# Kernel tuning notes

Hardware: AMD Instinct MI355X
Metric: run time of the kernel (lower is better)

Reference implementation:

```python
import jax, jax.numpy as jnp
import numpy as np
from jax import lax

KERNEL = 5  # cv2 np.ones((5,5)) structuring element
EDGE_WEIGHT = 0.1


def _edge_weights(target):
    # target: [B,1,H,W] float. Binary mask -> morphological gradient via
    # max-pool (dilate) and min-pool (erode) with 5x5 window, SAME padding.
    # cv2 pads dilate with -inf and erode with +inf, so padding never
    # creates or removes foreground; reduce_window init values match that.
    b = (target > 0.5).astype(target.dtype)
    win = (1, 1, KERNEL, KERNEL)
    ones = (1, 1, 1, 1)
    dilated = lax.reduce_window(b, jnp.float32(-jnp.inf), lax.max, win, ones, 'SAME')
    eroded = lax.reduce_window(b, jnp.float32(jnp.inf), lax.min, win, ones, 'SAME')
    edge = dilated - eroded
    # Samples with empty masks get edge==0 everywhere, so the per-sample
    # binary_mask.sum()>0 guard in the original is a no-op here.
    return jnp.where(edge > 0, jnp.float32(EDGE_WEIGHT), jnp.float32(1.0))


def setup_inputs() -> dict:
    key = jax.random.key(0)
    k1, k2 = jax.random.split(key)
    shape = (32, 1, 1024, 1024)
    pred = jax.random.normal(k1, shape, dtype=jnp.float32)
    target = jax.random.randint(k2, shape, 0, 2).astype(jnp.float32)
    return {"pred": pred, "target": target}


def reference(pred, target):
    # BCEWithLogitsLoss(reduction='none'): softplus(x) - x*t (stable form)
    loss = jax.nn.softplus(pred) - pred * target
    # Weighting branch only taken when target.max()==1 and target.min()==0
    cond = jnp.logical_and(target.max() == 1.0, target.min() == 0.0)
    weights = _edge_weights(target)
    weights = jnp.where(cond, weights, jnp.float32(1.0))
    return (loss * weights).mean()
```

## Files before the change

kernel.cpp:

```cpp
#include <hip/hip_runtime.h>


#define IMG  1024
#define RPW  8
#define NTOT 33554432.0

typedef unsigned long long u64;

__device__ __forceinline__ u64 shfl64(u64 v, int src) {
    unsigned lo = (unsigned)__shfl((int)(unsigned)(v & 0xffffffffULL), src, 64);
    unsigned hi = (unsigned)__shfl((int)(unsigned)(v >> 32), src, 64);
    return ((u64)hi << 32) | lo;
}
__device__ __forceinline__ u64 bcast64(u64 v, int srcImm) {
    unsigned lo = (unsigned)__builtin_amdgcn_readlane((int)(unsigned)(v & 0xffffffffULL), srcImm);
    unsigned hi = (unsigned)__builtin_amdgcn_readlane((int)(unsigned)(v >> 32), srcImm);
    return ((u64)hi << 32) | lo;
}

__device__ __forceinline__ unsigned encf(float f) {
    unsigned u = __float_as_uint(f);
    return (u & 0x80000000u) ? ~u : (u | 0x80000000u);
}
__device__ __forceinline__ float decf(unsigned e) {
    unsigned u = (e & 0x80000000u) ? (e & 0x7fffffffu) : ~e;
    return __uint_as_float(u);
}

__global__ void bbl_init(double* dws, unsigned* uws) {
    if (threadIdx.x == 0) {
        dws[0] = 0.0; dws[1] = 0.0;
        uws[0] = 0xFFFFFFFFu;
        uws[1] = 0u;
    }
}

__global__ __launch_bounds__(256) void bbl_main(
        const float* __restrict__ pred,
        const float* __restrict__ target,
        double* __restrict__ dws, unsigned* __restrict__ uws) {
    __shared__ float    redS1[4], redSe[4];
    __shared__ unsigned redMn[4], redMx[4];

    const int tid  = threadIdx.x;
    const int lane = tid & 63;
    const int wid  = tid >> 6;
    const int gw   = blockIdx.x * 4 + wid;
    const int img  = gw >> 7;
    const int r0   = (gw & 127) * RPW;
    const size_t base = (size_t)img * IMG * IMG;
    const float* tbase = target + base;
    const float* pbase = pred + base;

    const int w = lane & 15;
    const int k = w & 3;

    float vmin = 3.4e38f, vmax = -3.4e38f;
    float s1 = 0.f, se = 0.f;

    auto loadrow = [&](int gr, bool mm) -> u64 {
        const float4* rp = (const float4*)(tbase + (size_t)gr * IMG);
        u64 myw = 0ULL;
        #pragma unroll
        for (int it = 0; it < 4; ++it) {
            float4 v = rp[it * 64 + lane];
            if (mm) {
                vmin = fminf(vmin, fminf(fminf(v.x, v.y), fminf(v.z, v.w)));
                vmax = fmaxf(vmax, fmaxf(fmaxf(v.x, v.y), fmaxf(v.z, v.w)));
            }
            u64 b0 = __ballot(v.x > 0.5f);
            u64 b1 = __ballot(v.y > 0.5f);
            u64 b2 = __ballot(v.z > 0.5f);
            u64 b3 = __ballot(v.w > 0.5f);
            u64 bw = (k == 0) ? b0 : (k == 1) ? b1 : (k == 2) ? b2 : b3;
            if ((w >> 2) == it) myw = bw;
        }
        return myw;
    };

    u64 q0 = loadrow(max(r0 - 2, 0), false);
    u64 q1 = loadrow(max(r0 - 1, 0), false);
    u64 q2 = loadrow(r0, true);
    u64 q3 = loadrow(r0 + 1, true);

    for (int r = r0; r < r0 + RPW; ++r) {
        const int nr = min(r + 2, IMG - 1);
        u64 q4 = loadrow(nr, r + 2 <= r0 + RPW - 1);

        const float4* pp = (const float4*)(pbase + (size_t)r * IMG);
        float4 p0 = pp[0 * 64 + lane];
        float4 p1 = pp[1 * 64 + lane];
        float4 p2 = pp[2 * 64 + lane];
        float4 p3 = pp[3 * 64 + lane];

        u64 vd = q0 | q1 | q2 | q3 | q4;
        u64 ve = q0 & q1 & q2 & q3 & q4;
        u64 ct = q2;

        u64 hd = vd, he = ve;
        #pragma unroll
        for (int di = 0; di < 4; ++di) {
            const int d = (di < 2) ? di - 2 : di - 1;
            int wp = w + d;
            bool inp = (wp >= 0) && (wp < 16);
            u64 ad = shfl64(vd, wp & 15);
            u64 ae = shfl64(ve, wp & 15);
            ad = inp ? ad : 0ULL;
            ae = inp ? ae : ~0ULL;
            int ws2 = wp + ((d > 0) ? -4 : 4);
            u64 bd = shfl64(vd, ws2 & 15);
            u64 be = shfl64(ve, ws2 & 15);
            int kp = k + d;
            u64 rd, re;
            if (d > 0) {
                u64 wd = (bd >> 1) | (ad << 63);
                u64 we = (be >> 1) | (ae << 63);
                rd = (kp <= 3) ? ad : wd;
                re = (kp <= 3) ? ae : we;
            } else {
                u64 wd = (bd << 1) | (ad >> 63);
                u64 we = (be << 1) | (ae >> 63);
                rd = (kp >= 0) ? ad : wd;
                re = (kp >= 0) ? ae : we;
            }
            hd |= rd; he &= re;
        }
        u64 em = hd & ~he;

        #pragma unroll
        for (int it = 0; it < 4; ++it) {
            float4 p = (it == 0) ? p0 : (it == 1) ? p1 : (it == 2) ? p2 : p3;
            #pragma unroll
            for (int m = 0; m < 4; ++m) {
                u64 ew = bcast64(em, it * 4 + m);
                u64 tw = bcast64(ct, it * 4 + m);
                float x = (m == 0) ? p.x : (m == 1) ? p.y : (m == 2) ? p.z : p.w;
                unsigned tb = (unsigned)(tw >> lane) & 1u;
                unsigned eb = (unsigned)(ew >> lane) & 1u;
                float xt = tb ? x : 0.f;
                float sp = fmaxf(x, 0.f) + __logf(1.f + __expf(-fabsf(x)));
                float loss = sp - xt;
                s1 += loss;
                se += eb ? loss : 0.f;
            }
        }

        q0 = q1; q1 = q2; q2 = q3; q3 = q4;
    }

    for (int off = 32; off > 0; off >>= 1) {
        s1   += __shfl_down(s1, off);
        se   += __shfl_down(se, off);
        vmin  = fminf(vmin, __shfl_down(vmin, off));
        vmax  = fmaxf(vmax, __shfl_down(vmax, off));
    }
    if (lane == 0) {
        redS1[wid] = s1; redSe[wid] = se;
        redMn[wid] = encf(vmin); redMx[wid] = encf(vmax);
    }
    __syncthreads();
    if (tid == 0) {
        float S1 = 0.f, Se = 0.f; unsigned mn = 0xFFFFFFFFu, mx = 0u;
        #pragma unroll
        for (int i = 0; i < 4; ++i) {
            S1 += redS1[i]; Se += redSe[i];
            mn = min(mn, redMn[i]); mx = max(mx, redMx[i]);
        }
        atomicAdd(&dws[0], (double)S1);
        atomicAdd(&dws[1], (double)Se);
        atomicMin(&uws[0], mn);
        atomicMax(&uws[1], mx);
    }
}

__global__ void bbl_fin(const double* __restrict__ dws,
                        const unsigned* __restrict__ uws,
                        float* __restrict__ out) {
    if (threadIdx.x == 0) {
        float fmin = decf(uws[0]);
        float fmax = decf(uws[1]);
        bool cond = (fmax == 1.0f) && (fmin == 0.0f);
        double s = cond ? (dws[0] - 0.9 * dws[1]) : dws[0];
        out[0] = (float)(s / NTOT);
    }
}

extern "C" void kernel_launch(void* const* d_in, const int* in_sizes, int n_in,
                              void* d_out, int out_size, void* d_ws, size_t ws_size,
                              hipStream_t stream) {
    const float* pred   = (const float*)d_in[0];
    const float* target = (const float*)d_in[1];
    double*   dws = (double*)d_ws;
    unsigned* uws = (unsigned*)(dws + 2);
    float*    out = (float*)d_out;

    hipLaunchKernelGGL(bbl_init, dim3(1), dim3(64), 0, stream, dws, uws);
    hipLaunchKernelGGL(bbl_main, dim3(1024), dim3(256), 0, stream,
                       pred, target, dws, uws);
    hipLaunchKernelGGL(bbl_fin, dim3(1), dim3(64), 0, stream, dws, uws, out);
}
```

Before: 313.0 us.

## Split fused loss kernel into mask-pack, edge, and loss passes via workspace

Replaces the single fused kernel, which recomputed five rows of target ballots per output row, with three kernels. The first packs the target into a bitmask in workspace and reduces min/max. The second computes the 5x5 edge bitmask from the packed rows. The third streams pred together with both bitmasks to accumulate the loss. This removes the repeated halo reads of target and the cross-lane shuffles, at the cost of extra kernel launches and small workspace round trips, and keeps the original kernel as a fallback when the workspace is too small.

```diff
diff --git a/kernel.cpp b/kernel.cpp
--- a/kernel.cpp
+++ b/kernel.cpp
@@ -1,22 +1,12 @@
 #include <hip/hip_runtime.h>
 
 
-#define IMG  1024
-#define RPW  8
-#define NTOT 33554432.0
+#define IMG   1024
+#define NTOT  33554432.0
+#define NF4   8388608LL
+#define GRID  2048
 
 typedef unsigned long long u64;
-
-__device__ __forceinline__ u64 shfl64(u64 v, int src) {
-    unsigned lo = (unsigned)__shfl((int)(unsigned)(v & 0xffffffffULL), src, 64);
-    unsigned hi = (unsigned)__shfl((int)(unsigned)(v >> 32), src, 64);
-    return ((u64)hi << 32) | lo;
-}
-__device__ __forceinline__ u64 bcast64(u64 v, int srcImm) {
-    unsigned lo = (unsigned)__builtin_amdgcn_readlane((int)(unsigned)(v & 0xffffffffULL), srcImm);
-    unsigned hi = (unsigned)__builtin_amdgcn_readlane((int)(unsigned)(v >> 32), srcImm);
-    return ((u64)hi << 32) | lo;
-}
 
 __device__ __forceinline__ unsigned encf(float f) {
     unsigned u = __float_as_uint(f);
@@ -35,141 +25,124 @@
     }
 }
 
-__global__ __launch_bounds__(256) void bbl_main(
-        const float* __restrict__ pred,
-        const float* __restrict__ target,
-        double* __restrict__ dws, unsigned* __restrict__ uws) {
-    __shared__ float    redS1[4], redSe[4];
-    __shared__ unsigned redMn[4], redMx[4];
-
-    const int tid  = threadIdx.x;
-    const int lane = tid & 63;
-    const int wid  = tid >> 6;
-    const int gw   = blockIdx.x * 4 + wid;
-    const int img  = gw >> 7;
-    const int r0   = (gw & 127) * RPW;
-    const size_t base = (size_t)img * IMG * IMG;
-    const float* tbase = target + base;
-    const float* pbase = pred + base;
-
-    const int w = lane & 15;
-    const int k = w & 3;
-
+__global__ __launch_bounds__(256) void bbl_mask(
+        const float* __restrict__ target, u64* __restrict__ Bm,
+        unsigned* __restrict__ uws) {
+    __shared__ unsigned rmn[4], rmx[4];
+    const int tid = threadIdx.x, lane = tid & 63, wid = tid >> 6;
+    const long long stride = (long long)GRID * 256;
     float vmin = 3.4e38f, vmax = -3.4e38f;
-    float s1 = 0.f, se = 0.f;
-
-    auto loadrow = [&](int gr, bool mm) -> u64 {
-        const float4* rp = (const float4*)(tbase + (size_t)gr * IMG);
-        u64 myw = 0ULL;
-        #pragma unroll
-        for (int it = 0; it < 4; ++it) {
-            float4 v = rp[it * 64 + lane];
-            if (mm) {
-                vmin = fminf(vmin, fminf(fminf(v.x, v.y), fminf(v.z, v.w)));
-                vmax = fmaxf(vmax, fmaxf(fmaxf(v.x, v.y), fmaxf(v.z, v.w)));
-            }
-            u64 b0 = __ballot(v.x > 0.5f);
-            u64 b1 = __ballot(v.y > 0.5f);
-            u64 b2 = __ballot(v.z > 0.5f);
-            u64 b3 = __ballot(v.w > 0.5f);
-            u64 bw = (k == 0) ? b0 : (k == 1) ? b1 : (k == 2) ? b2 : b3;
-            if ((w >> 2) == it) myw = bw;
-        }
-        return myw;
-    };
-
-    u64 q0 = loadrow(max(r0 - 2, 0), false);
-    u64 q1 = loadrow(max(r0 - 1, 0), false);
-    u64 q2 = loadrow(r0, true);
-    u64 q3 = loadrow(r0 + 1, true);
-
-    for (int r = r0; r < r0 + RPW; ++r) {
-        const int nr = min(r + 2, IMG - 1);
-        u64 q4 = loadrow(nr, r + 2 <= r0 + RPW - 1);
-
-        const float4* pp = (const float4*)(pbase + (size_t)r * IMG);
-        float4 p0 = pp[0 * 64 + lane];
-        float4 p1 = pp[1 * 64 + lane];
-        float4 p2 = pp[2 * 64 + lane];
-        float4 p3 = pp[3 * 64 + lane];
-
-        u64 vd = q0 | q1 | q2 | q3 | q4;
-        u64 ve = q0 & q1 & q2 & q3 & q4;
-        u64 ct = q2;
-
-        u64 hd = vd, he = ve;
-        #pragma unroll
-        for (int di = 0; di < 4; ++di) {
-            const int d = (di < 2) ? di - 2 : di - 1;
-            int wp = w + d;
-            bool inp = (wp >= 0) && (wp < 16);
-            u64 ad = shfl64(vd, wp & 15);
-            u64 ae = shfl64(ve, wp & 15);
-            ad = inp ? ad : 0ULL;
-            ae = inp ? ae : ~0ULL;
-            int ws2 = wp + ((d > 0) ? -4 : 4);
-            u64 bd = shfl64(vd, ws2 & 15);
-            u64 be = shfl64(ve, ws2 & 15);
-            int kp = k + d;
-            u64 rd, re;
-            if (d > 0) {
-                u64 wd = (bd >> 1) | (ad << 63);
-                u64 we = (be >> 1) | (ae << 63);
-                rd = (kp <= 3) ? ad : wd;
-                re = (kp <= 3) ? ae : we;
-            } else {
-                u64 wd = (bd << 1) | (ad >> 63);
-                u64 we = (be << 1) | (ae >> 63);
-                rd = (kp >= 0) ? ad : wd;
-                re = (kp >= 0) ? ae : we;
-            }
-            hd |= rd; he &= re;
-        }
-        u64 em = hd & ~he;
-
-        #pragma unroll
-        for (int it = 0; it < 4; ++it) {
-            float4 p = (it == 0) ? p0 : (it == 1) ? p1 : (it == 2) ? p2 : p3;
-            #pragma unroll
-            for (int m = 0; m < 4; ++m) {
-                u64 ew = bcast64(em, it * 4 + m);
-                u64 tw = bcast64(ct, it * 4 + m);
-                float x = (m == 0) ? p.x : (m == 1) ? p.y : (m == 2) ? p.z : p.w;
-                unsigned tb = (unsigned)(tw >> lane) & 1u;
-                unsigned eb = (unsigned)(ew >> lane) & 1u;
-                float xt = tb ? x : 0.f;
-                float sp = fmaxf(x, 0.f) + __logf(1.f + __expf(-fabsf(x)));
-                float loss = sp - xt;
-                s1 += loss;
-                se += eb ? loss : 0.f;
-            }
-        }
-
-        q0 = q1; q1 = q2; q2 = q3; q3 = q4;
-    }
-
+
+    for (long long q = (long long)blockIdx.x * 256 + tid; q < NF4; q += stride) {
+        float4 v = ((const float4*)target)[q];
+        vmin = fminf(vmin, fminf(fminf(v.x, v.y), fminf(v.z, v.w)));
+        vmax = fmaxf(vmax, fmaxf(fmaxf(v.x, v.y), fmaxf(v.z, v.w)));
+        u64 b0 = __ballot(v.x > 0.5f);
+        u64 b1 = __ballot(v.y > 0.5f);
+        u64 b2 = __ballot(v.z > 0.5f);
+        u64 b3 = __ballot(v.w > 0.5f);
+        if (lane < 4) {
+            u64 val = (lane == 0) ? b0 : (lane == 1) ? b1 : (lane == 2) ? b2 : b3;
+            long long q0 = q - lane;
+            Bm[(q0 >> 4) + lane] = val;
+        }
+    }
     for (int off = 32; off > 0; off >>= 1) {
-        s1   += __shfl_down(s1, off);
-        se   += __shfl_down(se, off);
-        vmin  = fminf(vmin, __shfl_down(vmin, off));
-        vmax  = fmaxf(vmax, __shfl_down(vmax, off));
-    }
-    if (lane == 0) {
-        redS1[wid] = s1; redSe[wid] = se;
-        redMn[wid] = encf(vmin); redMx[wid] = encf(vmax);
-    }
+        vmin = fminf(vmin, __shfl_down(vmin, off));
+        vmax = fmaxf(vmax, __shfl_down(vmax, off));
+    }
+    if (lane == 0) { rmn[wid] = encf(vmin); rmx[wid] = encf(vmax); }
     __syncthreads();
     if (tid == 0) {
-        float S1 = 0.f, Se = 0.f; unsigned mn = 0xFFFFFFFFu, mx = 0u;
-        #pragma unroll
-        for (int i = 0; i < 4; ++i) {
-            S1 += redS1[i]; Se += redSe[i];
-            mn = min(mn, redMn[i]); mx = max(mx, redMx[i]);
-        }
+        unsigned mn = rmn[0], mx = rmx[0];
+        #pragma unroll
+        for (int i = 1; i < 4; ++i) { mn = min(mn, rmn[i]); mx = max(mx, rmx[i]); }
+        atomicMin(&uws[0], mn);
+        atomicMax(&uws[1], mx);
+    }
+}
+
+__global__ __launch_bounds__(256) void bbl_edge(
+        const u64* __restrict__ Bm, u64* __restrict__ Em) {
+    const int t  = blockIdx.x * 256 + threadIdx.x;
+    const int w  = t & 15;
+    const int rw = t >> 4;
+    const int r  = rw & 1023;
+    const u64* B = Bm + (((long long)(rw >> 10)) << 14);
+    const int lo = max(r - 2, 0), hi = min(r + 2, IMG - 1);
+
+    u64 vd[7], ve[7];
+    #pragma unroll
+    for (int j = 0; j < 7; ++j) {
+        const int wj = w - 3 + j;
+        if (wj < 0 || wj > 15) { vd[j] = 0ULL; ve[j] = ~0ULL; }
+        else {
+            u64 o = 0ULL, a = ~0ULL;
+            for (int g = lo; g <= hi; ++g) { u64 b = B[g * 16 + wj]; o |= b; a &= b; }
+            vd[j] = o; ve[j] = a;
+        }
+    }
+    const int k = w & 3;
+    u64 hd = vd[3], he = ve[3];
+    #pragma unroll
+    for (int di = 0; di < 4; ++di) {
+        const int d = (di < 2) ? di - 2 : di - 1;
+        const int kp = k + d;
+        u64 td, te;
+        if (kp >= 0 && kp <= 3) { td = vd[3 + d];                     te = ve[3 + d]; }
+        else if (kp > 3)        { td = (vd[3 + d - 4] >> 1) | (vd[3 + d] << 63);
+                                  te = (ve[3 + d - 4] >> 1) | (ve[3 + d] << 63); }
+        else                    { td = (vd[3 + d + 4] << 1) | (vd[3 + d] >> 63);
+                                  te = (ve[3 + d + 4] << 1) | (ve[3 + d] >> 63); }
+        hd |= td; he &= te;
+    }
+    Em[t] = hd & ~he;
+}
+
+__global__ __launch_bounds__(256) void bbl_loss(
+        const float* __restrict__ pred, const u64* __restrict__ Bm,
+        const u64* __restrict__ Em, double* __restrict__ dws) {
+    __shared__ float rs1[4], rse[4];
+    const int tid = threadIdx.x, lane = tid & 63, wid = tid >> 6;
+    const long long stride = (long long)GRID * 256;
+    float s1 = 0.f, se = 0.f;
+
+    for (long long q = (long long)blockIdx.x * 256 + tid; q < NF4; q += stride) {
+        float4 p = ((const float4*)pred)[q];
+        const long long wb = (q >> 6) << 2;
+        const int l = (int)(q & 63);
+        u64 t0 = Bm[wb + 0], t1 = Bm[wb + 1], t2 = Bm[wb + 2], t3 = Bm[wb + 3];
+        u64 e0 = Em[wb + 0], e1 = Em[wb + 1], e2 = Em[wb + 2], e3 = Em[wb + 3];
+        float x, loss;
+        x = p.x;
+        loss = fmaxf(x, 0.f) + __logf(1.f + __expf(-fabsf(x)))
+             - (((t0 >> l) & 1ULL) ? x : 0.f);
+        s1 += loss; se += ((e0 >> l) & 1ULL) ? loss : 0.f;
+        x = p.y;
+        loss = fmaxf(x, 0.f) + __logf(1.f + __expf(-fabsf(x)))
+             - (((t1 >> l) & 1ULL) ? x : 0.f);
+        s1 += loss; se += ((e1 >> l) & 1ULL) ? loss : 0.f;
+        x = p.z;
+        loss = fmaxf(x, 0.f) + __logf(1.f + __expf(-fabsf(x)))
+             - (((t2 >> l) & 1ULL) ? x : 0.f);
+        s1 += loss; se += ((e2 >> l) & 1ULL) ? loss : 0.f;
+        x = p.w;
+        loss = fmaxf(x, 0.f) + __logf(1.f + __expf(-fabsf(x)))
+             - (((t3 >> l) & 1ULL) ? x : 0.f);
+        s1 += loss; se += ((e3 >> l) & 1ULL) ? loss : 0.f;
+    }
+
+    for (int off = 32; off > 0; off >>= 1) {
+        s1 += __shfl_down(s1, off);
+        se += __shfl_down(se, off);
+    }
+    if (lane == 0) { rs1[wid] = s1; rse[wid] = se; }
+    __syncthreads();
+    if (tid == 0) {
+        float S1 = rs1[0] + rs1[1] + rs1[2] + rs1[3];
+        float Se = rse[0] + rse[1] + rse[2] + rse[3];
         atomicAdd(&dws[0], (double)S1);
         atomicAdd(&dws[1], (double)Se);
-        atomicMin(&uws[0], mn);
-        atomicMax(&uws[1], mx);
     }
 }
 
@@ -185,17 +158,145 @@
     }
 }
 
+__device__ __forceinline__ u64 shfl64(u64 v, int src) {
+    unsigned lo = (unsigned)__shfl((int)(unsigned)(v & 0xffffffffULL), src, 64);
+    unsigned hi = (unsigned)__shfl((int)(unsigned)(v >> 32), src, 64);
+    return ((u64)hi << 32) | lo;
+}
+__device__ __forceinline__ u64 bcast64(u64 v, int srcImm) {
+    unsigned lo = (unsigned)__builtin_amdgcn_readlane((int)(unsigned)(v & 0xffffffffULL), srcImm);
+    unsigned hi = (unsigned)__builtin_amdgcn_readlane((int)(unsigned)(v >> 32), srcImm);
+    return ((u64)hi << 32) | lo;
+}
+
+__global__ __launch_bounds__(256) void bbl_fallback(
+        const float* __restrict__ pred,
+        const float* __restrict__ target,
+        double* __restrict__ dws, unsigned* __restrict__ uws) {
+    __shared__ float    redS1[4], redSe[4];
+    __shared__ unsigned redMn[4], redMx[4];
+    const int tid = threadIdx.x, lane = tid & 63, wid = tid >> 6;
+    const int gw = blockIdx.x * 4 + wid;
+    const int img = gw >> 7;
+    const int r0 = (gw & 127) * 8;
+    const size_t base = (size_t)img * IMG * IMG;
+    const float* tbase = target + base;
+    const float* pbase = pred + base;
+    const int w = lane & 15, k = w & 3;
+    float vmin = 3.4e38f, vmax = -3.4e38f, s1 = 0.f, se = 0.f;
+
+    auto loadrow = [&](int gr, bool mm) -> u64 {
+        const float4* rp = (const float4*)(tbase + (size_t)gr * IMG);
+        u64 myw = 0ULL;
+        #pragma unroll
+        for (int it = 0; it < 4; ++it) {
+            float4 v = rp[it * 64 + lane];
+            if (mm) {
+                vmin = fminf(vmin, fminf(fminf(v.x, v.y), fminf(v.z, v.w)));
+                vmax = fmaxf(vmax, fmaxf(fmaxf(v.x, v.y), fmaxf(v.z, v.w)));
+            }
+            u64 b0 = __ballot(v.x > 0.5f), b1 = __ballot(v.y > 0.5f);
+            u64 b2 = __ballot(v.z > 0.5f), b3 = __ballot(v.w > 0.5f);
+            u64 bw = (k == 0) ? b0 : (k == 1) ? b1 : (k == 2) ? b2 : b3;
+            if ((w >> 2) == it) myw = bw;
+        }
+        return myw;
+    };
+
+    u64 q0 = loadrow(max(r0 - 2, 0), false);
+    u64 q1 = loadrow(max(r0 - 1, 0), false);
+    u64 q2 = loadrow(r0, true);
+    u64 q3 = loadrow(r0 + 1, true);
+
+    for (int r = r0; r < r0 + 8; ++r) {
+        const int nr = min(r + 2, IMG - 1);
+        u64 q4 = loadrow(nr, r + 2 <= r0 + 7);
+        const float4* pp = (const float4*)(pbase + (size_t)r * IMG);
+        float4 p0 = pp[0 * 64 + lane], p1 = pp[1 * 64 + lane];
+        float4 p2 = pp[2 * 64 + lane], p3 = pp[3 * 64 + lane];
+        u64 vd = q0 | q1 | q2 | q3 | q4;
+        u64 ve = q0 & q1 & q2 & q3 & q4;
+        u64 ct = q2, hd = vd, he = ve;
+        #pragma unroll
+        for (int di = 0; di < 4; ++di) {
+            const int d = (di < 2) ? di - 2 : di - 1;
+            int wp = w + d;
+            bool inp = (wp >= 0) && (wp < 16);
+            u64 ad = shfl64(vd, wp & 15), ae = shfl64(ve, wp & 15);
+            ad = inp ? ad : 0ULL; ae = inp ? ae : ~0ULL;
+            int ws2 = wp + ((d > 0) ? -4 : 4);
+            u64 bd = shfl64(vd, ws2 & 15), be = shfl64(ve, ws2 & 15);
+            int kp = k + d;
+            u64 rd, re;
+            if (d > 0) {
+                rd = (kp <= 3) ? ad : ((bd >> 1) | (ad << 63));
+                re = (kp <= 3) ? ae : ((be >> 1) | (ae << 63));
+            } else {
+                rd = (kp >= 0) ? ad : ((bd << 1) | (ad >> 63));
+                re = (kp >= 0) ? ae : ((be << 1) | (ae >> 63));
+            }
+            hd |= rd; he &= re;
+        }
+        u64 em = hd & ~he;
+        #pragma unroll
+        for (int it = 0; it < 4; ++it) {
+            float4 p = (it == 0) ? p0 : (it == 1) ? p1 : (it == 2) ? p2 : p3;
+            #pragma unroll
+            for (int m = 0; m < 4; ++m) {
+                u64 ew = bcast64(em, it * 4 + m);
+                u64 tw = bcast64(ct, it * 4 + m);
+                float x = (m == 0) ? p.x : (m == 1) ? p.y : (m == 2) ? p.z : p.w;
+                float xt = ((tw >> lane) & 1ULL) ? x : 0.f;
+                float loss = fmaxf(x, 0.f) + __logf(1.f + __expf(-fabsf(x))) - xt;
+                s1 += loss; se += ((ew >> lane) & 1ULL) ? loss : 0.f;
+            }
+        }
+        q0 = q1; q1 = q2; q2 = q3; q3 = q4;
+    }
+    for (int off = 32; off > 0; off >>= 1) {
+        s1 += __shfl_down(s1, off); se += __shfl_down(se, off);
+        vmin = fminf(vmin, __shfl_down(vmin, off));
+        vmax = fmaxf(vmax, __shfl_down(vmax, off));
+    }
+    if (lane == 0) {
+        redS1[wid] = s1; redSe[wid] = se;
+        redMn[wid] = encf(vmin); redMx[wid] = encf(vmax);
+    }
+    __syncthreads();
+    if (tid == 0) {
+        float S1 = 0.f, Se = 0.f; unsigned mn = 0xFFFFFFFFu, mx = 0u;
+        #pragma unroll
+        for (int i = 0; i < 4; ++i) {
+            S1 += redS1[i]; Se += redSe[i];
+            mn = min(mn, redMn[i]); mx = max(mx, redMx[i]);
+        }
+        atomicAdd(&dws[0], (double)S1); atomicAdd(&dws[1], (double)Se);
+        atomicMin(&uws[0], mn); atomicMax(&uws[1], mx);
+    }
+}
+
 extern "C" void kernel_launch(void* const* d_in, const int* in_sizes, int n_in,
                               void* d_out, int out_size, void* d_ws, size_t ws_size,
                               hipStream_t stream) {
     const float* pred   = (const float*)d_in[0];
     const float* target = (const float*)d_in[1];
     double*   dws = (double*)d_ws;
-    unsigned* uws = (unsigned*)(dws + 2);
+    unsigned* uws = (unsigned*)((char*)d_ws + 16);
     float*    out = (float*)d_out;
 
+    const size_t MASKB = 4194304;
+    const size_t need  = 4096 + 2 * MASKB;
+    u64* Bm = (u64*)((char*)d_ws + 4096);
+    u64* Em = (u64*)((char*)d_ws + 4096 + MASKB);
+
     hipLaunchKernelGGL(bbl_init, dim3(1), dim3(64), 0, stream, dws, uws);
-    hipLaunchKernelGGL(bbl_main, dim3(1024), dim3(256), 0, stream,
-                       pred, target, dws, uws);
+    if (ws_size >= need) {
+        hipLaunchKernelGGL(bbl_mask, dim3(GRID), dim3(256), 0, stream, target, Bm, uws);
+        hipLaunchKernelGGL(bbl_edge, dim3(GRID), dim3(256), 0, stream, Bm, Em);
+        hipLaunchKernelGGL(bbl_loss, dim3(GRID), dim3(256), 0, stream, pred, Bm, Em, dws);
+    } else {
+        hipLaunchKernelGGL(bbl_fallback, dim3(1024), dim3(256), 0, stream,
+                           pred, target, dws, uws);
+    }
     hipLaunchKernelGGL(bbl_fin, dim3(1), dim3(64), 0, stream, dws, uws, out);
 }
```

After: 352.1 us. +12.5%, slower.
